# Kernel tuning notes

Measured on AMD Instinct MI355X. Metric: run time of the kernel, lower is better.

The kernel has to match this reference:

```python
import jax, jax.numpy as jnp
import numpy as np

B, P, K, F, H = 128, 200, 60, 4, 64   # events, points/event, knn k, feat dim, hidden
N = B * P


def setup_inputs() -> dict:
    key = jax.random.key(0)
    k0, k1, k2, k3 = jax.random.split(key, 4)
    x = jax.random.normal(k0, (N, F), jnp.float32)
    pos = jax.random.normal(k1, (N, 3), jnp.float32)
    batch = jnp.arange(N, dtype=jnp.int32) // P  # sorted event ids, equal-size events
    W1 = jax.random.normal(k2, (F + 3, H), jnp.float32) / np.sqrt(F + 3)
    b1 = jnp.zeros((H,), jnp.float32)
    W2 = jax.random.normal(k3, (H, H), jnp.float32) / np.sqrt(H)
    b2 = jnp.zeros((H,), jnp.float32)
    return {"x": x, "pos": pos, "batch": batch, "W1": W1, "b1": b1, "W2": W2, "b2": b2}


def _knn_edges(pos):
    """knn_graph(pos, K, batch, loop=False, flow='source_to_target').
    Equal-size events -> batched [B,P,P] pairwise distances, no cross-event edges."""
    p = pos.reshape(B, P, 3)
    d2 = jnp.sum((p[:, :, None, :] - p[:, None, :, :]) ** 2, axis=-1)  # [B,P,P]
    d2 = d2 + jnp.eye(P, dtype=d2.dtype) * 1e10                        # exclude self (loop=False)
    _, nbr = jax.lax.top_k(-d2, K)                                     # [B,P,K] local neighbor ids
    src = (nbr + (jnp.arange(B, dtype=nbr.dtype) * P)[:, None, None]).reshape(-1)  # sources j
    dst = jnp.repeat(jnp.arange(N, dtype=src.dtype), K)                             # targets i
    return jnp.stack([src, dst])  # [2, N*K]


def _local_nn(m, W1, b1, W2, b2):
    h = jax.nn.relu(m @ W1 + b1)
    return jax.nn.relu(h @ W2 + b2)


def reference(x, pos, batch, W1, b1, W2, b2):
    edge_index = _knn_edges(pos)
    src, dst = edge_index[0], edge_index[1]
    # PointConv message: net(concat[x_j, pos_j - pos_i]) on each edge
    rel = pos[src] - pos[dst]                             # [E,3]
    m = jnp.concatenate([x[src], rel], axis=-1)           # [E,F+3]
    h = _local_nn(m, W1, b1, W2, b2)                      # [E,H]
    out = h.reshape(N, K, H).max(axis=1)                  # max-aggregate per target node
    # PyG PointConv adds self-loops by default: message with rel = 0
    m_self = jnp.concatenate([x, jnp.zeros((N, 3), x.dtype)], axis=-1)
    h_self = _local_nn(m_self, W1, b1, W2, b2)            # [N,H]
    out = jnp.maximum(out, h_self)
    return (out, pos, batch, edge_index)
```

## Files before the change

kernel.cpp:

```cpp
#include <hip/hip_runtime.h>
#include <hip/hip_bf16.h>

typedef unsigned int u32;
typedef unsigned long long u64;
typedef __attribute__((ext_vector_type(8))) short bf16x8;
typedef __attribute__((ext_vector_type(4))) float f32x4;
typedef __attribute__((ext_vector_type(4))) u32 u32x4;

#define NB 128
#define PP 200
#define KK 60
#define NN (NB*PP)
#define HH 64
#define TW 5
#define TB 20
#define BPE 10

#define OUT_OFF   0
#define POS_OFF   (NN*HH)
#define BATCH_OFF (POS_OFF + NN*3)
#define ESRC_OFF  (BATCH_OFF + NN)
#define EDST_OFF  (ESRC_OFF + NN*KK)

static __device__ __forceinline__ u32 packtr(float a, float b) {
    return __builtin_amdgcn_perm(__float_as_uint(b), __float_as_uint(a), 0x07060302u);
}
static __device__ __forceinline__ u32 prefix_lt(u64 b) {
    return __builtin_amdgcn_mbcnt_hi((u32)(b >> 32),
                                     __builtin_amdgcn_mbcnt_lo((u32)b, 0));
}

__global__ __launch_bounds__(256) void fused_kernel(const float* __restrict__ x,
                                                    const float* __restrict__ pos,
                                                    const float* __restrict__ W1,
                                                    const float* __restrict__ b1p,
                                                    const float* __restrict__ W2,
                                                    const float* __restrict__ b2p,
                                                    float* __restrict__ out) {
    __shared__ alignas(16) float xs[PP * 4];
    __shared__ alignas(16) float psl[PP * 3];
    __shared__ alignas(16) u32 jslot[4 * TW * 64];
    __shared__ alignas(16) u32 msg[4 * 256];
    __shared__ alignas(16) u32 pkW1[64 * 4];
    __shared__ alignas(16) u32 pkW2T[64 * 33];
    __shared__ alignas(16) float b2s[64];
    __shared__ alignas(16) u32 zrow[4];

    int tid = threadIdx.x, blk = blockIdx.x;
    int e = blk / BPE;
    int pl0b = (blk % BPE) * TB;
    int i0b  = e * PP + pl0b;

    if (tid < 200) ((f32x4*)xs)[tid]  = ((const f32x4*)x)[e * PP + tid];
    if (tid < 150) ((f32x4*)psl)[tid] = ((const f32x4*)pos)[e * 150 + tid];
    if (tid < 4)   zrow[tid] = 0u;

    {
        int m = tid & 63, d = tid >> 6;
        float hiv = (d < 3) ? W1[(2*d + 1)*64 + m] : b1p[m];
        pkW1[m*4 + d] = packtr(W1[(2*d)*64 + m], hiv);
    }
    #pragma unroll
    for (int r = 0; r < 4; ++r) {
        int g = r * 256 + tid;
        int kp = g >> 4, colq = g & 15;
        f32x4 ra = *(const f32x4*)&W2[(2*kp)    *64 + colq*4];
        f32x4 rb = *(const f32x4*)&W2[(2*kp + 1)*64 + colq*4];
        #pragma unroll
        for (int c = 0; c < 4; ++c)
            pkW2T[(colq*4 + c)*33 + kp] = packtr(ra[c], rb[c]);
    }
    if (tid < 64) b2s[tid] = b2p[tid];
    __syncthreads();

    if (tid < 3*TB) out[POS_OFF + i0b * 3 + tid] = psl[pl0b * 3 + tid];
    if (tid < TB)   out[BATCH_OFF + i0b + tid] = (float)e;

    int lane = tid & 63, wv = tid >> 6;
    int lo16 = lane & 15, hi16 = lane >> 4;
    int plW0 = pl0b + wv * TW;
    int iW0  = e * PP + plW0;

    u32 key[TW][4];
    {
        float ax[TW], ay[TW], az[TW];
        #pragma unroll
        for (int t = 0; t < TW; ++t) {
            ax[t] = psl[(plW0+t)*3]; ay[t] = psl[(plW0+t)*3+1]; az[t] = psl[(plW0+t)*3+2];
        }
        #pragma unroll
        for (int q = 0; q < 4; ++q) {
            int j = lane + q * 64;
            int jc = (j < PP) ? j : 0;
            float px = psl[jc*3], py = psl[jc*3+1], pz = psl[jc*3+2];
            #pragma unroll
            for (int t = 0; t < TW; ++t) {
                float dx = px-ax[t], dy = py-ay[t], dz = pz-az[t];
                float d2 = dx*dx + dy*dy + dz*dz;
                key[t][q] = (j < PP && j != plW0 + t)
                          ? ((__float_as_uint(d2) & 0xFFFFFF00u) | (u32)j) : 0xFFFFFFFFu;
            }
        }
    }

    u32 lo[TW], hi[TW]; int done[TW];
    #pragma unroll
    for (int t = 0; t < TW; ++t) { lo[t] = 0u; hi[t] = 0x7F800000u; done[t] = 0; }
    #pragma unroll 1
    for (int it = 0; it < 40; ++it) {
        #pragma unroll
        for (int t = 0; t < TW; ++t) {
            if (!done[t]) {
                u32 m = lo[t] + ((hi[t] - lo[t]) >> 1);
                int c = __builtin_popcountll(__ballot(key[t][0] < m))
                      + __builtin_popcountll(__ballot(key[t][1] < m))
                      + __builtin_popcountll(__ballot(key[t][2] < m))
                      + __builtin_popcountll(__ballot(key[t][3] < m));
                if (c >= KK) hi[t] = m; else lo[t] = m;
                done[t] = (c == KK) | (hi[t] - lo[t] <= 1u);
            }
        }
        int alldone = done[0];
        #pragma unroll
        for (int t = 1; t < TW; ++t) alldone &= done[t];
        if (alldone) break;
    }

    const int jsb = wv * (TW * 64);
    #pragma unroll
    for (int t = 0; t < TW; ++t) {
        if (lane >= KK) jslot[jsb + t * 64 + lane] = (u32)(plW0 + t);
        u64 m0 = __ballot(key[t][0] < hi[t]);
        u64 m1 = __ballot(key[t][1] < hi[t]);
        u64 m2 = __ballot(key[t][2] < hi[t]);
        u64 m3 = __ballot(key[t][3] < hi[t]);
        u32 s1 = (u32)__builtin_popcountll(m0);
        u32 s2 = s1 + (u32)__builtin_popcountll(m1);
        u32 s3 = s2 + (u32)__builtin_popcountll(m2);
        u32 sl[4] = { prefix_lt(m0), s1 + prefix_lt(m1),
                      s2 + prefix_lt(m2), s3 + prefix_lt(m3) };
        #pragma unroll
        for (int q = 0; q < 4; ++q)
            if (key[t][q] < hi[t]) jslot[jsb + t * 64 + (int)sl[q]] = key[t][q] & 0xFFu;
    }
    #pragma unroll
    for (int t = 0; t < TW; ++t) {
        int i = iW0 + t;
        if (lane < KK) {
            out[ESRC_OFF + i * KK + lane] = (float)(e * PP + (int)jslot[jsb + t * 64 + lane]);
            out[EDST_OFF + i * KK + lane] = (float)i;
        }
    }

    bf16x8 w1f[4];
    #pragma unroll
    for (int th = 0; th < 4; ++th) {
        union { u32 w[4]; bf16x8 v; } u;
        if (hi16 == 0) *(u32x4*)u.w = *(const u32x4*)&pkW1[(th * 16 + lo16) * 4];
        else { u.w[0] = u.w[1] = u.w[2] = u.w[3] = 0u; }
        w1f[th] = u.v;
    }
    bf16x8 bfr[4][2];
    #pragma unroll
    for (int t = 0; t < 4; ++t)
        #pragma unroll
        for (int s = 0; s < 2; ++s) {
            union { u32 w[4]; bf16x8 v; } u;
            int base = (t * 16 + lo16) * 33 + s * 16 + hi16 * 4;
            #pragma unroll
            for (int d = 0; d < 4; ++d) u.w[d] = pkW2T[base + d];
            bfr[t][s] = u.v;
        }
    float b2me = b2s[lane];

    const int msb = wv * 256;
    const u32* mbase = (hi16 == 0) ? &msg[msb + lo16 * 4] : zrow;
    const int mstep  = (hi16 == 0) ? 64 : 0;

    for (int tl = 0; tl < TW; ++tl) {
        int i = iW0 + tl, pl = plW0 + tl;
        int jloc = (int)jslot[jsb + tl * 64 + lane];
        f32x4 xv = ((const f32x4*)xs)[jloc];
        float rx = psl[jloc*3]   - psl[pl*3];
        float ry = psl[jloc*3+1] - psl[pl*3+1];
        float rz = psl[jloc*3+2] - psl[pl*3+2];
        u32x4 mrow;
        mrow[0] = packtr(xv[0], xv[1]);
        mrow[1] = packtr(xv[2], xv[3]);
        mrow[2] = packtr(rx, ry);
        mrow[3] = packtr(rz, 1.0f);
        *(u32x4*)&msg[msb + lane * 4] = mrow;

        float rmax[4] = {-3.0e38f, -3.0e38f, -3.0e38f, -3.0e38f};
        #pragma unroll
        for (int rt = 0; rt < 4; ++rt) {
            union { u32 w[4]; bf16x8 v; } mu;
            *(u32x4*)mu.w = *(const u32x4*)(mbase + rt * mstep);

            f32x4 c1[4];
            #pragma unroll
            for (int th = 0; th < 4; ++th)
                c1[th] = __builtin_amdgcn_mfma_f32_16x16x32_bf16(w1f[th], mu.v,
                                                                 (f32x4)0.f, 0, 0, 0);
            f32x4 acc[4];
            #pragma unroll
            for (int t = 0; t < 4; ++t) acc[t] = (f32x4)0.f;

            #pragma unroll
            for (int s = 0; s < 2; ++s) {
                u32 pe0 = packtr(fmaxf(c1[2*s][0], 0.f), fmaxf(c1[2*s][1], 0.f));
                u32 pe1 = packtr(fmaxf(c1[2*s][2], 0.f), fmaxf(c1[2*s][3], 0.f));
                u32 po0 = packtr(fmaxf(c1[2*s+1][0], 0.f), fmaxf(c1[2*s+1][1], 0.f));
                u32 po1 = packtr(fmaxf(c1[2*s+1][2], 0.f), fmaxf(c1[2*s+1][3], 0.f));
                union { u32 w[4]; bf16x8 v; } u;
                {
                    auto t0 = __builtin_amdgcn_permlane32_swap(pe0, po0, false, false);
                    auto w0 = __builtin_amdgcn_permlane16_swap(t0[0], t0[1], false, false);
                    u.w[0] = w0[0]; u.w[2] = w0[1];
                }
                {
                    auto t1 = __builtin_amdgcn_permlane32_swap(pe1, po1, false, false);
                    auto w1 = __builtin_amdgcn_permlane16_swap(t1[0], t1[1], false, false);
                    u.w[1] = w1[0]; u.w[3] = w1[1];
                }
                #pragma unroll
                for (int t = 0; t < 4; ++t)
                    acc[t] = __builtin_amdgcn_mfma_f32_16x16x32_bf16(u.v, bfr[t][s],
                                                                     acc[t], 0, 0, 0);
            }
            #pragma unroll
            for (int t = 0; t < 4; ++t) {
                rmax[t] = fmaxf(fmaxf(acc[t][0], acc[t][1]), rmax[t]);
                rmax[t] = fmaxf(fmaxf(acc[t][2], acc[t][3]), rmax[t]);
            }
        }
        #pragma unroll
        for (int t = 0; t < 4; ++t) {
            rmax[t] = fmaxf(rmax[t], __shfl_xor(rmax[t], 16, 64));
            rmax[t] = fmaxf(rmax[t], __shfl_xor(rmax[t], 32, 64));
        }
        float sel = rmax[0];
        sel = (hi16 == 1) ? rmax[1] : sel;
        sel = (hi16 == 2) ? rmax[2] : sel;
        sel = (hi16 == 3) ? rmax[3] : sel;
        out[OUT_OFF + i * 64 + lane] = fmaxf(sel + b2me, 0.f);
    }
}

extern "C" void kernel_launch(void* const* d_in, const int* in_sizes, int n_in,
                              void* d_out, int out_size, void* d_ws, size_t ws_size,
                              hipStream_t stream) {
    const float* x     = (const float*)d_in[0];
    const float* pos   = (const float*)d_in[1];
    const float* W1    = (const float*)d_in[3];
    const float* b1    = (const float*)d_in[4];
    const float* W2    = (const float*)d_in[5];
    const float* b2    = (const float*)d_in[6];
    float* out = (float*)d_out;
    (void)d_ws; (void)ws_size; (void)in_sizes; (void)n_in; (void)out_size;

    fused_kernel<<<dim3(NN / TB), dim3(256), 0, stream>>>(x, pos, W1, b1, W2, b2, out);
}
```

Baseline: 115.3 us.

## Reshape work split to 5 waves x 2 targets, batch messages, use permlane reductions

Changes the block from 4 waves handling 5 targets each to 5 waves handling 2 targets each. Blocks per event go from 10 to 20 and the grid doubles, which spreads the kNN and MLP work across more waves. Message rows for all of a wave's targets are now built before the MFMA loop, which is fully unrolled and wrapped in s_setprio. The cross-lane max uses permlane16/32 swaps instead of shfl_xor, and the pos/batch copy-out moves before the barrier and reads global memory directly. The cost is that W1/W2 repacking into LDS is repeated per block, twice as often as before, and LDS use rises for the per-target message buffers.

```diff
diff --git a/kernel.cpp b/kernel.cpp
--- a/kernel.cpp
+++ b/kernel.cpp
@@ -12,9 +12,11 @@
 #define KK 60
 #define NN (NB*PP)
 #define HH 64
-#define TW 5
-#define TB 20
-#define BPE 10
+#define TW 2
+#define NWV 5
+#define TB (TW*NWV)
+#define BPE (PP/TB)
+#define NTHREADS (NWV*64)
 
 #define OUT_OFF   0
 #define POS_OFF   (NN*HH)
@@ -29,8 +31,16 @@
     return __builtin_amdgcn_mbcnt_hi((u32)(b >> 32),
                                      __builtin_amdgcn_mbcnt_lo((u32)b, 0));
 }
-
-__global__ __launch_bounds__(256) void fused_kernel(const float* __restrict__ x,
+static __device__ __forceinline__ float wavemax16(float v) {
+    u32 x = __float_as_uint(v);
+    auto p16 = __builtin_amdgcn_permlane16_swap(x, x, false, false);
+    float m = fmaxf(__uint_as_float(p16[0]), __uint_as_float(p16[1]));
+    u32 y = __float_as_uint(m);
+    auto p32 = __builtin_amdgcn_permlane32_swap(y, y, false, false);
+    return fmaxf(__uint_as_float(p32[0]), __uint_as_float(p32[1]));
+}
+
+__global__ __launch_bounds__(NTHREADS) void fused_kernel(const float* __restrict__ x,
                                                     const float* __restrict__ pos,
                                                     const float* __restrict__ W1,
                                                     const float* __restrict__ b1p,
@@ -39,8 +49,8 @@
                                                     float* __restrict__ out) {
     __shared__ alignas(16) float xs[PP * 4];
     __shared__ alignas(16) float psl[PP * 3];
-    __shared__ alignas(16) u32 jslot[4 * TW * 64];
-    __shared__ alignas(16) u32 msg[4 * 256];
+    __shared__ alignas(16) u32 jslot[NWV * TW * 64];
+    __shared__ alignas(16) u32 msg[NWV * TW * 256];
     __shared__ alignas(16) u32 pkW1[64 * 4];
     __shared__ alignas(16) u32 pkW2T[64 * 33];
     __shared__ alignas(16) float b2s[64];
@@ -51,30 +61,32 @@
     int pl0b = (blk % BPE) * TB;
     int i0b  = e * PP + pl0b;
 
+    if (tid < 3*TB) out[POS_OFF + i0b * 3 + tid] = pos[i0b * 3 + tid];
+    if (tid < TB)   out[BATCH_OFF + i0b + tid] = (float)e;
+
     if (tid < 200) ((f32x4*)xs)[tid]  = ((const f32x4*)x)[e * PP + tid];
     if (tid < 150) ((f32x4*)psl)[tid] = ((const f32x4*)pos)[e * 150 + tid];
     if (tid < 4)   zrow[tid] = 0u;
 
-    {
+    if (tid < 256) {
         int m = tid & 63, d = tid >> 6;
         float hiv = (d < 3) ? W1[(2*d + 1)*64 + m] : b1p[m];
         pkW1[m*4 + d] = packtr(W1[(2*d)*64 + m], hiv);
     }
     #pragma unroll
     for (int r = 0; r < 4; ++r) {
-        int g = r * 256 + tid;
-        int kp = g >> 4, colq = g & 15;
-        f32x4 ra = *(const f32x4*)&W2[(2*kp)    *64 + colq*4];
-        f32x4 rb = *(const f32x4*)&W2[(2*kp + 1)*64 + colq*4];
-        #pragma unroll
-        for (int c = 0; c < 4; ++c)
-            pkW2T[(colq*4 + c)*33 + kp] = packtr(ra[c], rb[c]);
+        int g = r * NTHREADS + tid;
+        if (g < 1024) {
+            int kp = g >> 4, colq = g & 15;
+            f32x4 ra = *(const f32x4*)&W2[(2*kp)    *64 + colq*4];
+            f32x4 rb = *(const f32x4*)&W2[(2*kp + 1)*64 + colq*4];
+            #pragma unroll
+            for (int c = 0; c < 4; ++c)
+                pkW2T[(colq*4 + c)*33 + kp] = packtr(ra[c], rb[c]);
+        }
     }
     if (tid < 64) b2s[tid] = b2p[tid];
     __syncthreads();
-
-    if (tid < 3*TB) out[POS_OFF + i0b * 3 + tid] = psl[pl0b * 3 + tid];
-    if (tid < TB)   out[BATCH_OFF + i0b + tid] = (float)e;
 
     int lane = tid & 63, wv = tid >> 6;
     int lo16 = lane & 15, hi16 = lane >> 4;
@@ -173,12 +185,10 @@
         }
     float b2me = b2s[lane];
 
-    const int msb = wv * 256;
-    const u32* mbase = (hi16 == 0) ? &msg[msb + lo16 * 4] : zrow;
-    const int mstep  = (hi16 == 0) ? 64 : 0;
-
+    const int msb = wv * (TW * 256);
+    #pragma unroll
     for (int tl = 0; tl < TW; ++tl) {
-        int i = iW0 + tl, pl = plW0 + tl;
+        int pl = plW0 + tl;
         int jloc = (int)jslot[jsb + tl * 64 + lane];
         f32x4 xv = ((const f32x4*)xs)[jloc];
         float rx = psl[jloc*3]   - psl[pl*3];
@@ -189,9 +199,17 @@
         mrow[1] = packtr(xv[2], xv[3]);
         mrow[2] = packtr(rx, ry);
         mrow[3] = packtr(rz, 1.0f);
-        *(u32x4*)&msg[msb + lane * 4] = mrow;
+        *(u32x4*)&msg[msb + tl * 256 + lane * 4] = mrow;
+    }
+
+    #pragma unroll
+    for (int tl = 0; tl < TW; ++tl) {
+        int i = iW0 + tl;
+        const u32* mbase = (hi16 == 0) ? &msg[msb + tl * 256 + lo16 * 4] : zrow;
+        const int mstep  = (hi16 == 0) ? 64 : 0;
 
         float rmax[4] = {-3.0e38f, -3.0e38f, -3.0e38f, -3.0e38f};
+        __builtin_amdgcn_s_setprio(1);
         #pragma unroll
         for (int rt = 0; rt < 4; ++rt) {
             union { u32 w[4]; bf16x8 v; } mu;
@@ -234,11 +252,9 @@
                 rmax[t] = fmaxf(fmaxf(acc[t][2], acc[t][3]), rmax[t]);
             }
         }
-        #pragma unroll
-        for (int t = 0; t < 4; ++t) {
-            rmax[t] = fmaxf(rmax[t], __shfl_xor(rmax[t], 16, 64));
-            rmax[t] = fmaxf(rmax[t], __shfl_xor(rmax[t], 32, 64));
-        }
+        __builtin_amdgcn_s_setprio(0);
+        #pragma unroll
+        for (int t = 0; t < 4; ++t) rmax[t] = wavemax16(rmax[t]);
         float sel = rmax[0];
         sel = (hi16 == 1) ? rmax[1] : sel;
         sel = (hi16 == 2) ? rmax[2] : sel;
@@ -259,5 +275,5 @@
     float* out = (float*)d_out;
     (void)d_ws; (void)ws_size; (void)in_sizes; (void)n_in; (void)out_size;
 
-    fused_kernel<<<dim3(NN / TB), dim3(256), 0, stream>>>(x, pos, W1, b1, W2, b2, out);
-}
+    fused_kernel<<<dim3(NN / TB), dim3(NTHREADS), 0, stream>>>(x, pos, W1, b1, W2, b2, out);
+}
```

Measured after the change: 127.2 us. 10.3% more time.
